# Performance work log

Measured on AMD Instinct MI355X. Metric: run time of the kernel, lower is better.

Reference implementation:

```python
import jax, jax.numpy as jnp
import numpy as np


def setup_inputs() -> dict:
    key = jax.random.key(0)
    ks = jax.random.split(key, 7)
    B, S, D_IN, D_K, D_V = 4, 4096, 1024, 64, 64
    s = 1.0 / np.sqrt(D_IN)
    return {
        "query": jax.random.normal(ks[0], (B, S, D_IN), jnp.float32),
        "key": jax.random.normal(ks[1], (B, S, D_IN), jnp.float32),
        "value": jax.random.normal(ks[2], (B, S, D_IN), jnp.float32),
        "Wq": jax.random.normal(ks[3], (D_IN, D_K), jnp.float32) * s,
        "bq": jnp.zeros((D_K,), jnp.float32),
        "Wk": jax.random.normal(ks[4], (D_IN, D_K), jnp.float32) * s,
        "bk": jnp.zeros((D_K,), jnp.float32),
        "Wv": jax.random.normal(ks[5], (D_IN, D_V), jnp.float32) * s,
        "bv": jnp.zeros((D_V,), jnp.float32),
    }


def reference(query, key, value, Wq, bq, Wk, bk, Wv, bv):
    # q(query) is computed twice in the original but is identical; compute once.
    q = query @ Wq + bq            # [B,S,dk]
    k = key @ Wk + bk              # [B,S,dk]
    v = value @ Wv + bv            # [B,S,dv]
    scale = jnp.asarray(q.shape[-1] ** 0.5, q.dtype)
    scores = jnp.einsum("bqd,bkd->bqk", q, k) / scale  # [B,S,S]
    probs = jax.nn.softmax(scores, axis=-1)
    return jnp.einsum("bqk,bkd->bqd", probs, v)        # [B,S,dv]
```

## Files before the change

### kernel.cpp

```cpp
#include <hip/hip_runtime.h>
#include <cmath>

constexpr int B_  = 4;
constexpr int S_  = 4096;
constexpr int DIN = 1024;
constexpr int DH  = 64;

typedef short bf16x8 __attribute__((ext_vector_type(8)));
typedef float f32x4  __attribute__((ext_vector_type(4)));

__device__ __forceinline__ ushort f2bf(float x) {
    unsigned int u = __float_as_uint(x);
    return (ushort)((u + 0x7FFFu + ((u >> 16) & 1u)) >> 16);
}

__global__ __launch_bounds__(256) void proj_kernel(
    const float* __restrict__ Xq, const float* __restrict__ Xk, const float* __restrict__ Xv,
    const float* __restrict__ Wq, const float* __restrict__ Wk, const float* __restrict__ Wv,
    const float* __restrict__ bq, const float* __restrict__ bk, const float* __restrict__ bv,
    ushort* __restrict__ Qb, ushort* __restrict__ Kb, ushort* __restrict__ Vt)
{
    const float *X, *W, *bias;
    if (blockIdx.y == 0)      { X = Xq; W = Wq; bias = bq; }
    else if (blockIdx.y == 1) { X = Xk; W = Wk; bias = bk; }
    else                      { X = Xv; W = Wv; bias = bv; }

    __shared__ ushort Xs[64 * 72];
    __shared__ ushort Wt[64 * 72];

    const int tid  = threadIdx.x;
    const int w    = tid >> 6;
    const int lane = tid & 63;
    const int m    = lane & 15;
    const int quad = lane >> 4;
    const int row0 = blockIdx.x * 64;

    float bias_v[4];
    #pragma unroll
    for (int nt = 0; nt < 4; ++nt) bias_v[nt] = bias[nt * 16 + m];

    f32x4 acc[4] = {};

    for (int kk = 0; kk < DIN; kk += 64) {
        for (int i = tid; i < 1024; i += 256) {
            const int r = i >> 4, c = (i & 15) << 2;
            const float4 f = *(const float4*)(X + (size_t)(row0 + r) * DIN + kk + c);
            ushort4 h;
            h.x = f2bf(f.x); h.y = f2bf(f.y); h.z = f2bf(f.z); h.w = f2bf(f.w);
            *(ushort4*)&Xs[r * 72 + c] = h;
        }
        for (int i = tid; i < 1024; i += 256) {
            const int k = i >> 4, n4 = (i & 15) << 2;
            const float4 f = *(const float4*)(W + (size_t)(kk + k) * DH + n4);
            Wt[(n4 + 0) * 72 + k] = f2bf(f.x);
            Wt[(n4 + 1) * 72 + k] = f2bf(f.y);
            Wt[(n4 + 2) * 72 + k] = f2bf(f.z);
            Wt[(n4 + 3) * 72 + k] = f2bf(f.w);
        }
        __syncthreads();
        #pragma unroll
        for (int ks = 0; ks < 2; ++ks) {
            const bf16x8 a = *(const bf16x8*)&Xs[(w * 16 + m) * 72 + ks * 32 + quad * 8];
            #pragma unroll
            for (int nt = 0; nt < 4; ++nt) {
                const bf16x8 bfr = *(const bf16x8*)&Wt[(nt * 16 + m) * 72 + ks * 32 + quad * 8];
                acc[nt] = __builtin_amdgcn_mfma_f32_16x16x32_bf16(a, bfr, acc[nt], 0, 0, 0);
            }
        }
        __syncthreads();
    }

    if (blockIdx.y < 2) {
        ushort* Out = (blockIdx.y == 0) ? Qb : Kb;
        const float sc = (blockIdx.y == 0) ? 0.125f : 1.0f;
        #pragma unroll
        for (int nt = 0; nt < 4; ++nt)
            #pragma unroll
            for (int j = 0; j < 4; ++j) {
                const int row = row0 + w * 16 + quad * 4 + j;
                Out[(size_t)row * DH + nt * 16 + m] = f2bf((acc[nt][j] + bias_v[nt]) * sc);
            }
    } else {
        __syncthreads();
        #pragma unroll
        for (int nt = 0; nt < 4; ++nt)
            #pragma unroll
            for (int j = 0; j < 4; ++j) {
                const int d = nt * 16 + m;
                const int s = w * 16 + quad * 4 + j;
                Xs[d * 72 + s] = f2bf(acc[nt][j] + bias_v[nt]);
            }
        __syncthreads();
        const int batch = row0 >> 12;
        const int s0    = row0 & 4095;
        for (int i = tid; i < 512; i += 256) {
            const int d = i >> 3, c = i & 7;
            const uint4 v = *(const uint4*)&Xs[d * 72 + c * 8];
            *(uint4*)(Vt + ((size_t)batch * 64 + d) * S_ + s0 + c * 8) = v;
        }
    }
}

__global__ __launch_bounds__(256) void attn_kernel(
    const ushort* __restrict__ Qb, const ushort* __restrict__ Kb,
    const ushort* __restrict__ Vt, float* __restrict__ Opart, float* __restrict__ Lpart)
{
    __shared__ ushort Ks[64 * 64];
    __shared__ ushort Vs[64 * 64];
    __shared__ ushort Pt[128 * 72];

    const int tid  = threadIdx.x;
    const int w    = tid >> 6;
    const int lane = tid & 63;
    const int m    = lane & 15;
    const int quad = lane >> 4;
    const int b    = blockIdx.z, jc = blockIdx.y, qt = blockIdx.x;
    const int q0   = qt * 128;

    bf16x8 qf[2][2];
    #pragma unroll
    for (int rt = 0; rt < 2; ++rt)
        #pragma unroll
        for (int ks = 0; ks < 2; ++ks)
            qf[rt][ks] = *(const bf16x8*)(Qb + (size_t)(b * S_ + q0 + w * 32 + rt * 16 + m) * 64
                                             + ks * 32 + quad * 8);

    f32x4 acc_o[2][4] = {};
    float Lp[2][4] = {};

    const ushort* kbase = Kb + (size_t)b * S_ * 64;
    const ushort* vbase = Vt + (size_t)b * 64 * S_;

    for (int it = 0; it < 16; ++it) {
        const int jt = jc * 16 + it;
        __syncthreads();
        #pragma unroll
        for (int i = 0; i < 2; ++i) {
            const int slot = w * 128 + i * 64 + lane;
            const int j = slot >> 3, c = slot & 7;
            const ushort* gk = kbase + (size_t)(jt * 64 + j) * 64 + ((c ^ (j & 7)) * 8);
            __builtin_amdgcn_global_load_lds(
                (const __attribute__((address_space(1))) unsigned int*)gk,
                (__attribute__((address_space(3))) unsigned int*)&Ks[(w * 128 + i * 64) * 8],
                16, 0, 0);
            const ushort* gv = vbase + (size_t)j * S_ + jt * 64 + ((c ^ (j & 7)) * 8);
            __builtin_amdgcn_global_load_lds(
                (const __attribute__((address_space(1))) unsigned int*)gv,
                (__attribute__((address_space(3))) unsigned int*)&Vs[(w * 128 + i * 64) * 8],
                16, 0, 0);
        }
        __syncthreads();

        f32x4 acc_s[2][4] = {};
        #pragma unroll
        for (int ks = 0; ks < 2; ++ks)
            #pragma unroll
            for (int jt4 = 0; jt4 < 4; ++jt4) {
                const int j = jt4 * 16 + m;
                const bf16x8 kf = *(const bf16x8*)&Ks[j * 64 + (((ks * 4 + quad) ^ (j & 7)) * 8)];
                #pragma unroll
                for (int rt = 0; rt < 2; ++rt)
                    acc_s[rt][jt4] = __builtin_amdgcn_mfma_f32_16x16x32_bf16(
                        qf[rt][ks], kf, acc_s[rt][jt4], 0, 0, 0);
            }

        #pragma unroll
        for (int rt = 0; rt < 2; ++rt)
            #pragma unroll
            for (int jt4 = 0; jt4 < 4; ++jt4)
                #pragma unroll
                for (int r = 0; r < 4; ++r) {
                    const float e = __expf(acc_s[rt][jt4][r]);
                    Lp[rt][r] += e;
                    Pt[(w * 32 + rt * 16 + quad * 4 + r) * 72 + jt4 * 16 + m] = f2bf(e);
                }

        #pragma unroll
        for (int jc2 = 0; jc2 < 2; ++jc2) {
            bf16x8 pf[2];
            #pragma unroll
            for (int rt = 0; rt < 2; ++rt)
                pf[rt] = *(const bf16x8*)&Pt[(w * 32 + rt * 16 + m) * 72 + jc2 * 32 + quad * 8];
            #pragma unroll
            for (int dt = 0; dt < 4; ++dt) {
                const int d = dt * 16 + m;
                const bf16x8 vf = *(const bf16x8*)&Vs[d * 64 + (((jc2 * 4 + quad) ^ (d & 7)) * 8)];
                #pragma unroll
                for (int rt = 0; rt < 2; ++rt)
                    acc_o[rt][dt] = __builtin_amdgcn_mfma_f32_16x16x32_bf16(
                        pf[rt], vf, acc_o[rt][dt], 0, 0, 0);
            }
        }
    }

    #pragma unroll
    for (int rt = 0; rt < 2; ++rt)
        #pragma unroll
        for (int r = 0; r < 4; ++r) {
            float s = Lp[rt][r];
            #pragma unroll
            for (int off = 1; off < 16; off <<= 1)
                s += __shfl_xor(s, off, 64);
            Lp[rt][r] = s;
        }

    const size_t bj = (size_t)(b * 4 + jc);
    float* Ob = Opart + (bj << 18);
    #pragma unroll
    for (int rt = 0; rt < 2; ++rt) {
        #pragma unroll
        for (int dt = 0; dt < 4; ++dt)
            #pragma unroll
            for (int r = 0; r < 4; ++r) {
                const int row = q0 + w * 32 + rt * 16 + quad * 4 + r;
                Ob[(size_t)row * 64 + dt * 16 + m] = acc_o[rt][dt][r];
            }
        if (m == 0) {
            #pragma unroll
            for (int r = 0; r < 4; ++r)
                Lpart[bj * 4096 + q0 + w * 32 + rt * 16 + quad * 4 + r] = Lp[rt][r];
        }
    }
}

__global__ __launch_bounds__(256) void reduce_kernel(
    const float* __restrict__ Opart, const float* __restrict__ Lpart, float* __restrict__ out)
{
    const int g    = blockIdx.x * 256 + threadIdx.x;
    const int base = g << 2;
    const int b    = base >> 18;
    const int rem  = base & 0x3FFFF;
    const int q    = rem >> 6;
    float4 o = make_float4(0.f, 0.f, 0.f, 0.f);
    float  l = 0.f;
    #pragma unroll
    for (int jcc = 0; jcc < 4; ++jcc) {
        const float4 p = *(const float4*)(Opart + (((size_t)(b * 4 + jcc)) << 18) + rem);
        o.x += p.x; o.y += p.y; o.z += p.z; o.w += p.w;
        l += Lpart[(size_t)(b * 4 + jcc) * 4096 + q];
    }
    const float inv = 1.0f / l;
    o.x *= inv; o.y *= inv; o.z *= inv; o.w *= inv;
    *(float4*)(out + base) = o;
}

extern "C" void kernel_launch(void* const* d_in, const int* in_sizes, int n_in,
                              void* d_out, int out_size, void* d_ws, size_t ws_size,
                              hipStream_t stream)
{
    const float* query = (const float*)d_in[0];
    const float* key_  = (const float*)d_in[1];
    const float* value = (const float*)d_in[2];
    const float* Wq    = (const float*)d_in[3];
    const float* bq    = (const float*)d_in[4];
    const float* Wk    = (const float*)d_in[5];
    const float* bk    = (const float*)d_in[6];
    const float* Wv    = (const float*)d_in[7];
    const float* bv    = (const float*)d_in[8];
    float* out = (float*)d_out;

    char* ws = (char*)d_ws;
    ushort* Qb    = (ushort*)(ws);
    ushort* Kb    = (ushort*)(ws + (2  << 20));
    ushort* Vt    = (ushort*)(ws + (4  << 20));
    float*  Opart = (float*) (ws + (6  << 20));
    float*  Lpart = (float*) (ws + (22 << 20));

    proj_kernel<<<dim3(256, 3), 256, 0, stream>>>(
        query, key_, value, Wq, Wk, Wv, bq, bk, bv, Qb, Kb, Vt);
    attn_kernel<<<dim3(32, 4, 4), 256, 0, stream>>>(Qb, Kb, Vt, Opart, Lpart);
    reduce_kernel<<<dim3(1024), 256, 0, stream>>>(Opart, Lpart, out);
}
```

Before: 301.0 us.

## Pre-transpose weights, pipeline projection loads, halve attention q-tile, use exp2

A new setup kernel converts the weights to bf16 once per call into a pre-transposed, swizzled layout. The projection kernel then streams those weights into double-buffered LDS with global_load_lds and holds activations in registers with one-step-ahead prefetch, instead of converting both operands into LDS every step. The attention kernel halves its query tile to 64 rows per block, doubling the grid for more parallelism, and sets launch_bounds occupancy to 4. It also folds log2(e) into the Q scale so exp2f replaces __expf. The extra launch and the Wt_g buffer aliasing Opart are the main new costs and risks, though they look sequentially safe.

```diff
diff --git a/kernel.cpp b/kernel.cpp
--- a/kernel.cpp
+++ b/kernel.cpp
@@ -9,24 +9,54 @@
 typedef short bf16x8 __attribute__((ext_vector_type(8)));
 typedef float f32x4  __attribute__((ext_vector_type(4)));
 
+#define GPTR(p) (const __attribute__((address_space(1))) unsigned int*)(p)
+#define LPTR(p) (__attribute__((address_space(3))) unsigned int*)(p)
+
 __device__ __forceinline__ ushort f2bf(float x) {
     unsigned int u = __float_as_uint(x);
     return (ushort)((u + 0x7FFFu + ((u >> 16) & 1u)) >> 16);
 }
 
+__device__ __forceinline__ bf16x8 cvt8(float4 a, float4 b) {
+    union { bf16x8 v; ushort u[8]; } r;
+    r.u[0] = f2bf(a.x); r.u[1] = f2bf(a.y); r.u[2] = f2bf(a.z); r.u[3] = f2bf(a.w);
+    r.u[4] = f2bf(b.x); r.u[5] = f2bf(b.y); r.u[6] = f2bf(b.z); r.u[7] = f2bf(b.w);
+    return r.v;
+}
+
+#define QSCALE 0.18033688011112042f
+
+__global__ __launch_bounds__(256) void setup_w(
+    const float* __restrict__ Wq, const float* __restrict__ Wk,
+    const float* __restrict__ Wv, ushort* __restrict__ Wt_g)
+{
+    const int y = blockIdx.y;
+    const float* W = (y == 0) ? Wq : (y == 1) ? Wk : Wv;
+    const int g   = blockIdx.x * 256 + threadIdx.x;
+    const int p   = g & 7;
+    const int n   = (g >> 3) & 63;
+    const int win = g >> 9;
+    const int c   = p ^ (n & 7);
+    const int k0  = win * 64 + c * 8;
+    union { uint4 q; ushort u[8]; } r;
+    #pragma unroll
+    for (int i = 0; i < 8; ++i) r.u[i] = f2bf(W[(size_t)(k0 + i) * DH + n]);
+    *(uint4*)(Wt_g + ((size_t)y << 16) + (size_t)(((win * 64 + n) * 8 + p) * 8)) = r.q;
+}
+
 __global__ __launch_bounds__(256) void proj_kernel(
     const float* __restrict__ Xq, const float* __restrict__ Xk, const float* __restrict__ Xv,
-    const float* __restrict__ Wq, const float* __restrict__ Wk, const float* __restrict__ Wv,
     const float* __restrict__ bq, const float* __restrict__ bk, const float* __restrict__ bv,
+    const ushort* __restrict__ Wt_g,
     ushort* __restrict__ Qb, ushort* __restrict__ Kb, ushort* __restrict__ Vt)
 {
-    const float *X, *W, *bias;
-    if (blockIdx.y == 0)      { X = Xq; W = Wq; bias = bq; }
-    else if (blockIdx.y == 1) { X = Xk; W = Wk; bias = bk; }
-    else                      { X = Xv; W = Wv; bias = bv; }
-
-    __shared__ ushort Xs[64 * 72];
-    __shared__ ushort Wt[64 * 72];
+    const int y = blockIdx.y;
+    const float *X, *bias;
+    if (y == 0)      { X = Xq; bias = bq; }
+    else if (y == 1) { X = Xk; bias = bk; }
+    else             { X = Xv; bias = bv; }
+
+    __shared__ ushort Wlds[2][4096];
 
     const int tid  = threadIdx.x;
     const int w    = tid >> 6;
@@ -35,44 +65,62 @@
     const int quad = lane >> 4;
     const int row0 = blockIdx.x * 64;
 
+    const size_t  xrow = (size_t)(row0 + w * 16 + m) * DIN;
+    const ushort* wsrc = Wt_g + ((size_t)y << 16);
+
     float bias_v[4];
     #pragma unroll
     for (int nt = 0; nt < 4; ++nt) bias_v[nt] = bias[nt * 16 + m];
 
     f32x4 acc[4] = {};
 
-    for (int kk = 0; kk < DIN; kk += 64) {
-        for (int i = tid; i < 1024; i += 256) {
-            const int r = i >> 4, c = (i & 15) << 2;
-            const float4 f = *(const float4*)(X + (size_t)(row0 + r) * DIN + kk + c);
-            ushort4 h;
-            h.x = f2bf(f.x); h.y = f2bf(f.y); h.z = f2bf(f.z); h.w = f2bf(f.w);
-            *(ushort4*)&Xs[r * 72 + c] = h;
-        }
-        for (int i = tid; i < 1024; i += 256) {
-            const int k = i >> 4, n4 = (i & 15) << 2;
-            const float4 f = *(const float4*)(W + (size_t)(kk + k) * DH + n4);
-            Wt[(n4 + 0) * 72 + k] = f2bf(f.x);
-            Wt[(n4 + 1) * 72 + k] = f2bf(f.y);
-            Wt[(n4 + 2) * 72 + k] = f2bf(f.z);
-            Wt[(n4 + 3) * 72 + k] = f2bf(f.w);
+    #pragma unroll
+    for (int i = 0; i < 2; ++i) {
+        const int chunk = w * 2 + i;
+        __builtin_amdgcn_global_load_lds(GPTR(wsrc + chunk * 512 + lane * 8),
+                                         LPTR(&Wlds[0][chunk * 512]), 16, 0, 0);
+    }
+    float4 cur[4], nxt[4];
+    {
+        const float* px = X + xrow + quad * 8;
+        cur[0] = *(const float4*)(px);      cur[1] = *(const float4*)(px + 4);
+        cur[2] = *(const float4*)(px + 32); cur[3] = *(const float4*)(px + 36);
+    }
+    __syncthreads();
+
+    for (int it = 0; it < 16; ++it) {
+        if (it < 15) {
+            #pragma unroll
+            for (int i = 0; i < 2; ++i) {
+                const int chunk = w * 2 + i;
+                __builtin_amdgcn_global_load_lds(
+                    GPTR(wsrc + (it + 1) * 4096 + chunk * 512 + lane * 8),
+                    LPTR(&Wlds[(it + 1) & 1][chunk * 512]), 16, 0, 0);
+            }
+            const float* px = X + xrow + (it + 1) * 64 + quad * 8;
+            nxt[0] = *(const float4*)(px);      nxt[1] = *(const float4*)(px + 4);
+            nxt[2] = *(const float4*)(px + 32); nxt[3] = *(const float4*)(px + 36);
+        }
+        const ushort* buf = Wlds[it & 1];
+        #pragma unroll
+        for (int ks = 0; ks < 2; ++ks) {
+            const bf16x8 a = cvt8(cur[ks * 2], cur[ks * 2 + 1]);
+            #pragma unroll
+            for (int nt = 0; nt < 4; ++nt) {
+                const int n = nt * 16 + m;
+                const int p = (ks * 4 + quad) ^ (m & 7);
+                const bf16x8 bfr = *(const bf16x8*)&buf[n * 64 + p * 8];
+                acc[nt] = __builtin_amdgcn_mfma_f32_16x16x32_bf16(a, bfr, acc[nt], 0, 0, 0);
+            }
         }
         __syncthreads();
         #pragma unroll
-        for (int ks = 0; ks < 2; ++ks) {
-            const bf16x8 a = *(const bf16x8*)&Xs[(w * 16 + m) * 72 + ks * 32 + quad * 8];
-            #pragma unroll
-            for (int nt = 0; nt < 4; ++nt) {
-                const bf16x8 bfr = *(const bf16x8*)&Wt[(nt * 16 + m) * 72 + ks * 32 + quad * 8];
-                acc[nt] = __builtin_amdgcn_mfma_f32_16x16x32_bf16(a, bfr, acc[nt], 0, 0, 0);
-            }
-        }
-        __syncthreads();
-    }
-
-    if (blockIdx.y < 2) {
-        ushort* Out = (blockIdx.y == 0) ? Qb : Kb;
-        const float sc = (blockIdx.y == 0) ? 0.125f : 1.0f;
+        for (int i = 0; i < 4; ++i) cur[i] = nxt[i];
+    }
+
+    if (y < 2) {
+        ushort* Out = (y == 0) ? Qb : Kb;
+        const float sc = (y == 0) ? QSCALE : 1.0f;
         #pragma unroll
         for (int nt = 0; nt < 4; ++nt)
             #pragma unroll
@@ -81,33 +129,33 @@
                 Out[(size_t)row * DH + nt * 16 + m] = f2bf((acc[nt][j] + bias_v[nt]) * sc);
             }
     } else {
-        __syncthreads();
+        ushort* Vx = (ushort*)Wlds;
         #pragma unroll
         for (int nt = 0; nt < 4; ++nt)
             #pragma unroll
             for (int j = 0; j < 4; ++j) {
                 const int d = nt * 16 + m;
                 const int s = w * 16 + quad * 4 + j;
-                Xs[d * 72 + s] = f2bf(acc[nt][j] + bias_v[nt]);
+                Vx[d * 72 + (((s >> 3) ^ (d & 7)) * 8) + (s & 7)] = f2bf(acc[nt][j] + bias_v[nt]);
             }
         __syncthreads();
         const int batch = row0 >> 12;
         const int s0    = row0 & 4095;
         for (int i = tid; i < 512; i += 256) {
             const int d = i >> 3, c = i & 7;
-            const uint4 v = *(const uint4*)&Xs[d * 72 + c * 8];
+            const uint4 v = *(const uint4*)&Vx[d * 72 + ((c ^ (d & 7)) * 8)];
             *(uint4*)(Vt + ((size_t)batch * 64 + d) * S_ + s0 + c * 8) = v;
         }
     }
 }
 
-__global__ __launch_bounds__(256) void attn_kernel(
+__global__ __launch_bounds__(256, 4) void attn_kernel(
     const ushort* __restrict__ Qb, const ushort* __restrict__ Kb,
     const ushort* __restrict__ Vt, float* __restrict__ Opart, float* __restrict__ Lpart)
 {
     __shared__ ushort Ks[64 * 64];
     __shared__ ushort Vs[64 * 64];
-    __shared__ ushort Pt[128 * 72];
+    __shared__ ushort Pt[64 * 72];
 
     const int tid  = threadIdx.x;
     const int w    = tid >> 6;
@@ -115,18 +163,16 @@
     const int m    = lane & 15;
     const int quad = lane >> 4;
     const int b    = blockIdx.z, jc = blockIdx.y, qt = blockIdx.x;
-    const int q0   = qt * 128;
-
-    bf16x8 qf[2][2];
-    #pragma unroll
-    for (int rt = 0; rt < 2; ++rt)
-        #pragma unroll
-        for (int ks = 0; ks < 2; ++ks)
-            qf[rt][ks] = *(const bf16x8*)(Qb + (size_t)(b * S_ + q0 + w * 32 + rt * 16 + m) * 64
-                                             + ks * 32 + quad * 8);
-
-    f32x4 acc_o[2][4] = {};
-    float Lp[2][4] = {};
+    const int q0   = qt * 64;
+
+    bf16x8 qf[2];
+    #pragma unroll
+    for (int ks = 0; ks < 2; ++ks)
+        qf[ks] = *(const bf16x8*)(Qb + (size_t)(b * S_ + q0 + w * 16 + m) * 64
+                                     + ks * 32 + quad * 8);
+
+    f32x4 acc_o[4] = {};
+    float Lp[4] = {};
 
     const ushort* kbase = Kb + (size_t)b * S_ * 64;
     const ushort* vbase = Vt + (size_t)b * 64 * S_;
@@ -138,88 +184,69 @@
         for (int i = 0; i < 2; ++i) {
             const int slot = w * 128 + i * 64 + lane;
             const int j = slot >> 3, c = slot & 7;
-            const ushort* gk = kbase + (size_t)(jt * 64 + j) * 64 + ((c ^ (j & 7)) * 8);
             __builtin_amdgcn_global_load_lds(
-                (const __attribute__((address_space(1))) unsigned int*)gk,
-                (__attribute__((address_space(3))) unsigned int*)&Ks[(w * 128 + i * 64) * 8],
-                16, 0, 0);
-            const ushort* gv = vbase + (size_t)j * S_ + jt * 64 + ((c ^ (j & 7)) * 8);
+                GPTR(kbase + (size_t)(jt * 64 + j) * 64 + ((c ^ (j & 7)) * 8)),
+                LPTR(&Ks[(w * 128 + i * 64) * 8]), 16, 0, 0);
             __builtin_amdgcn_global_load_lds(
-                (const __attribute__((address_space(1))) unsigned int*)gv,
-                (__attribute__((address_space(3))) unsigned int*)&Vs[(w * 128 + i * 64) * 8],
-                16, 0, 0);
+                GPTR(vbase + (size_t)j * S_ + jt * 64 + ((c ^ (j & 7)) * 8)),
+                LPTR(&Vs[(w * 128 + i * 64) * 8]), 16, 0, 0);
         }
         __syncthreads();
 
-        f32x4 acc_s[2][4] = {};
+        f32x4 acc_s[4] = {};
         #pragma unroll
         for (int ks = 0; ks < 2; ++ks)
             #pragma unroll
             for (int jt4 = 0; jt4 < 4; ++jt4) {
                 const int j = jt4 * 16 + m;
                 const bf16x8 kf = *(const bf16x8*)&Ks[j * 64 + (((ks * 4 + quad) ^ (j & 7)) * 8)];
-                #pragma unroll
-                for (int rt = 0; rt < 2; ++rt)
-                    acc_s[rt][jt4] = __builtin_amdgcn_mfma_f32_16x16x32_bf16(
-                        qf[rt][ks], kf, acc_s[rt][jt4], 0, 0, 0);
-            }
-
-        #pragma unroll
-        for (int rt = 0; rt < 2; ++rt)
-            #pragma unroll
-            for (int jt4 = 0; jt4 < 4; ++jt4)
-                #pragma unroll
-                for (int r = 0; r < 4; ++r) {
-                    const float e = __expf(acc_s[rt][jt4][r]);
-                    Lp[rt][r] += e;
-                    Pt[(w * 32 + rt * 16 + quad * 4 + r) * 72 + jt4 * 16 + m] = f2bf(e);
-                }
+                acc_s[jt4] = __builtin_amdgcn_mfma_f32_16x16x32_bf16(
+                    qf[ks], kf, acc_s[jt4], 0, 0, 0);
+            }
+
+        #pragma unroll
+        for (int jt4 = 0; jt4 < 4; ++jt4)
+            #pragma unroll
+            for (int r = 0; r < 4; ++r) {
+                const float e = exp2f(acc_s[jt4][r]);
+                Lp[r] += e;
+                Pt[(w * 16 + quad * 4 + r) * 72 + jt4 * 16 + m] = f2bf(e);
+            }
 
         #pragma unroll
         for (int jc2 = 0; jc2 < 2; ++jc2) {
-            bf16x8 pf[2];
-            #pragma unroll
-            for (int rt = 0; rt < 2; ++rt)
-                pf[rt] = *(const bf16x8*)&Pt[(w * 32 + rt * 16 + m) * 72 + jc2 * 32 + quad * 8];
+            const bf16x8 pf = *(const bf16x8*)&Pt[(w * 16 + m) * 72 + jc2 * 32 + quad * 8];
             #pragma unroll
             for (int dt = 0; dt < 4; ++dt) {
                 const int d = dt * 16 + m;
                 const bf16x8 vf = *(const bf16x8*)&Vs[d * 64 + (((jc2 * 4 + quad) ^ (d & 7)) * 8)];
-                #pragma unroll
-                for (int rt = 0; rt < 2; ++rt)
-                    acc_o[rt][dt] = __builtin_amdgcn_mfma_f32_16x16x32_bf16(
-                        pf[rt], vf, acc_o[rt][dt], 0, 0, 0);
-            }
-        }
-    }
-
-    #pragma unroll
-    for (int rt = 0; rt < 2; ++rt)
-        #pragma unroll
-        for (int r = 0; r < 4; ++r) {
-            float s = Lp[rt][r];
-            #pragma unroll
-            for (int off = 1; off < 16; off <<= 1)
-                s += __shfl_xor(s, off, 64);
-            Lp[rt][r] = s;
-        }
+                acc_o[dt] = __builtin_amdgcn_mfma_f32_16x16x32_bf16(pf, vf, acc_o[dt], 0, 0, 0);
+            }
+        }
+    }
+
+    #pragma unroll
+    for (int r = 0; r < 4; ++r) {
+        float s = Lp[r];
+        #pragma unroll
+        for (int off = 1; off < 16; off <<= 1)
+            s += __shfl_xor(s, off, 64);
+        Lp[r] = s;
+    }
 
     const size_t bj = (size_t)(b * 4 + jc);
     float* Ob = Opart + (bj << 18);
     #pragma unroll
-    for (int rt = 0; rt < 2; ++rt) {
-        #pragma unroll
-        for (int dt = 0; dt < 4; ++dt)
-            #pragma unroll
-            for (int r = 0; r < 4; ++r) {
-                const int row = q0 + w * 32 + rt * 16 + quad * 4 + r;
-                Ob[(size_t)row * 64 + dt * 16 + m] = acc_o[rt][dt][r];
-            }
-        if (m == 0) {
-            #pragma unroll
-            for (int r = 0; r < 4; ++r)
-                Lpart[bj * 4096 + q0 + w * 32 + rt * 16 + quad * 4 + r] = Lp[rt][r];
-        }
+    for (int dt = 0; dt < 4; ++dt)
+        #pragma unroll
+        for (int r = 0; r < 4; ++r) {
+            const int row = q0 + w * 16 + quad * 4 + r;
+            Ob[(size_t)row * 64 + dt * 16 + m] = acc_o[dt][r];
+        }
+    if (m == 0) {
+        #pragma unroll
+        for (int r = 0; r < 4; ++r)
+            Lpart[bj * 4096 + q0 + w * 16 + quad * 4 + r] = Lp[r];
     }
 }
 
@@ -265,9 +292,11 @@
     ushort* Vt    = (ushort*)(ws + (4  << 20));
     float*  Opart = (float*) (ws + (6  << 20));
     float*  Lpart = (float*) (ws + (22 << 20));
-
+    ushort* Wt_g  = (ushort*)(ws + (6  << 20));
+
+    setup_w<<<dim3(32, 3), 256, 0, stream>>>(Wq, Wk, Wv, Wt_g);
     proj_kernel<<<dim3(256, 3), 256, 0, stream>>>(
-        query, key_, value, Wq, Wk, Wv, bq, bk, bv, Qb, Kb, Vt);
-    attn_kernel<<<dim3(32, 4, 4), 256, 0, stream>>>(Qb, Kb, Vt, Opart, Lpart);
+        query, key_, value, bq, bk, bv, Wt_g, Qb, Kb, Vt);
+    attn_kernel<<<dim3(64, 4, 4), 256, 0, stream>>>(Qb, Kb, Vt, Opart, Lpart);
     reduce_kernel<<<dim3(1024), 256, 0, stream>>>(Opart, Lpart, out);
 }
```

Result: faster. 265.0 us (-12.0%).
